# Optimization experiments

Measured on AMD Instinct MI355X. Metric: run time of the kernel, lower is better.

Reference implementation:

```python
import jax, jax.numpy as jnp
import numpy as np

EPS = 1e-05
NUM_SEGMENTS = 8  # number of point clouds packed along N


def setup_inputs() -> dict:
    key = jax.random.key(0)
    N, C = 1048576, 64
    seg_len = N // NUM_SEGMENTS
    x = jax.random.normal(key, (1, N, C), dtype=jnp.float32)
    # CSR offsets of equal-length contiguous segments: [0, L, 2L, ..., N]
    batch_offsets = (jnp.arange(NUM_SEGMENTS + 1, dtype=jnp.int32) * seg_len)
    # per-point segment id, consistent with offsets (segment-sorted)
    batch_indices = jnp.repeat(jnp.arange(NUM_SEGMENTS, dtype=jnp.int32), seg_len)
    weight = jnp.ones((C,), dtype=jnp.float32)
    bias_val = jnp.zeros((C,), dtype=jnp.float32)
    return {"x": x, "weight": weight, "bias_val": bias_val,
            "batch_offsets": batch_offsets, "batch_indices": batch_indices}


def reference(x, weight, bias_val, batch_offsets, batch_indices):
    # x: [B, N, C]; batch_offsets: [S+1]; batch_indices: [N]
    counts = (batch_offsets[1:] - batch_offsets[:-1]).astype(x.dtype)  # [S]

    def norm_one(xb):  # xb: [N, C]
        seg_mean = jax.ops.segment_sum(xb, batch_indices,
                                       num_segments=NUM_SEGMENTS) / counts[:, None]  # [S, C]
        centered = xb - seg_mean[batch_indices]                                      # [N, C]
        seg_var = jax.ops.segment_sum(centered * centered, batch_indices,
                                      num_segments=NUM_SEGMENTS) / counts[:, None]   # [S, C]
        std = jnp.sqrt(seg_var + EPS)                                                # [S, C]
        return centered / std[batch_indices]

    y = jax.vmap(norm_one)(x)  # [B, N, C]
    return y * weight + bias_val
```

## Files before the change

### kernel.cpp

```cpp
#include <hip/hip_runtime.h>
#include <hip/hip_bf16.h>


#define EPS 1e-5f

typedef float f32x4 __attribute__((ext_vector_type(4)));

__global__ __launch_bounds__(256) void pin_stats(
    const float4* __restrict__ x4, float* __restrict__ partials,
    int ppb, long N) {
    const int tid   = threadIdx.x;
    const int lane  = tid & 63;
    const int wave  = tid >> 6;
    const int cgrp  = lane & 15;
    const int quart = lane >> 4;
    const long bchunk = (long)gridDim.x - 1 - blockIdx.x;
    const long block_start = bchunk * ppb;

    float4 s = make_float4(0.f, 0.f, 0.f, 0.f);
    float4 q = make_float4(0.f, 0.f, 0.f, 0.f);

    const int iters = ppb >> 4;
    const long lane_base = (block_start + wave * 4 + quart) * 16 + cgrp;

    if (block_start + ppb <= N) {
        const int half = iters >> 1;
        float4 s1 = make_float4(0.f, 0.f, 0.f, 0.f);
        float4 q1 = make_float4(0.f, 0.f, 0.f, 0.f);
        #pragma unroll 4
        for (int it = 0; it < half; ++it) {
            float4 a = x4[lane_base + (long)it * 256];
            float4 b = x4[lane_base + (long)(it + half) * 256];
            s.x  += a.x; s.y  += a.y; s.z  += a.z; s.w  += a.w;
            q.x  += a.x * a.x; q.y  += a.y * a.y; q.z  += a.z * a.z; q.w  += a.w * a.w;
            s1.x += b.x; s1.y += b.y; s1.z += b.z; s1.w += b.w;
            q1.x += b.x * b.x; q1.y += b.y * b.y; q1.z += b.z * b.z; q1.w += b.w * b.w;
        }
        s.x += s1.x; s.y += s1.y; s.z += s1.z; s.w += s1.w;
        q.x += q1.x; q.y += q1.y; q.z += q1.z; q.w += q1.w;
    } else {
        for (int it = 0; it < iters; ++it) {
            long p = block_start + (long)it * 16 + wave * 4 + quart;
            if (p < N) {
                float4 v = x4[p * 16 + cgrp];
                s.x += v.x; s.y += v.y; s.z += v.z; s.w += v.w;
                q.x += v.x * v.x; q.y += v.y * v.y; q.z += v.z * v.z; q.w += v.w * v.w;
            }
        }
    }

    #pragma unroll
    for (int off = 16; off <= 32; off <<= 1) {
        s.x += __shfl_xor(s.x, off); s.y += __shfl_xor(s.y, off);
        s.z += __shfl_xor(s.z, off); s.w += __shfl_xor(s.w, off);
        q.x += __shfl_xor(q.x, off); q.y += __shfl_xor(q.y, off);
        q.z += __shfl_xor(q.z, off); q.w += __shfl_xor(q.w, off);
    }

    __shared__ float lds[4][16][8];
    if (lane < 16) {
        lds[wave][lane][0] = s.x; lds[wave][lane][1] = s.y;
        lds[wave][lane][2] = s.z; lds[wave][lane][3] = s.w;
        lds[wave][lane][4] = q.x; lds[wave][lane][5] = q.y;
        lds[wave][lane][6] = q.z; lds[wave][lane][7] = q.w;
    }
    __syncthreads();

    if (tid < 128) {
        int stat = tid >> 6;
        int ch   = tid & 63;
        int cg   = ch >> 2;
        int j    = ch & 3;
        float v = lds[0][cg][stat * 4 + j] + lds[1][cg][stat * 4 + j]
                + lds[2][cg][stat * 4 + j] + lds[3][cg][stat * 4 + j];
        partials[bchunk * 128 + tid] = v;
    }
}

__global__ __launch_bounds__(256) void pin_scale(
    const float* __restrict__ partials,
    const float* __restrict__ weight, const float* __restrict__ bias,
    const int* __restrict__ offs,
    float* __restrict__ scale, float* __restrict__ shift, int ppb) {
    const int s = blockIdx.x;
    const int c = threadIdx.x & 63;
    const int r = threadIdx.x >> 6;
    const int b0 = offs[s] / ppb;
    const int b1 = offs[s + 1] / ppb;

    float sum = 0.f, sq = 0.f;
    for (int blk = b0 + r; blk < b1; blk += 4) {
        sum += partials[(long)blk * 128 + c];
        sq  += partials[(long)blk * 128 + 64 + c];
    }

    __shared__ float lsum[4][64];
    __shared__ float lsq[4][64];
    lsum[r][c] = sum;
    lsq[r][c]  = sq;
    __syncthreads();

    if (r == 0) {
        float tsum = ((lsum[0][c] + lsum[1][c]) + lsum[2][c]) + lsum[3][c];
        float tsq  = ((lsq[0][c]  + lsq[1][c])  + lsq[2][c])  + lsq[3][c];
        float cnt  = (float)(offs[s + 1] - offs[s]);
        float mean = tsum / cnt;
        float var  = tsq / cnt - mean * mean;
        float sc   = weight[c] * rsqrtf(var + EPS);
        scale[s * 64 + c] = sc;
        shift[s * 64 + c] = bias[c] - mean * sc;
    }
}

#define K3_THREADS 256
#define K3_ITERS 16
__global__ __launch_bounds__(K3_THREADS) void pin_norm(
    const f32x4* __restrict__ x4, const int* __restrict__ bidx,
    const float4* __restrict__ scale4, const float4* __restrict__ shift4,
    f32x4* __restrict__ y4, long total4) {
    const long chunk = (long)blockIdx.x * (K3_THREADS * K3_ITERS);
    const int  tid   = threadIdx.x;
    const long p0    = chunk >> 4;
    const int  seg   = bidx[p0];
    const int  cgrp  = tid & 15;

    const float4 sc = scale4[seg * 16 + cgrp];
    const float4 sh = shift4[seg * 16 + cgrp];

    if (chunk + K3_THREADS * K3_ITERS <= total4) {
        #pragma unroll
        for (int k = 0; k < K3_ITERS; ++k) {
            long i = chunk + (long)k * K3_THREADS + tid;
            f32x4 v = x4[i];
            f32x4 o;
            o.x = v.x * sc.x + sh.x;
            o.y = v.y * sc.y + sh.y;
            o.z = v.z * sc.z + sh.z;
            o.w = v.w * sc.w + sh.w;
            __builtin_nontemporal_store(o, &y4[i]);
        }
    } else {
        for (int k = 0; k < K3_ITERS; ++k) {
            long i = chunk + (long)k * K3_THREADS + tid;
            if (i < total4) {
                f32x4 v = x4[i];
                f32x4 o;
                o.x = v.x * sc.x + sh.x;
                o.y = v.y * sc.y + sh.y;
                o.z = v.z * sc.z + sh.z;
                o.w = v.w * sc.w + sh.w;
                __builtin_nontemporal_store(o, &y4[i]);
            }
        }
    }
}

extern "C" void kernel_launch(void* const* d_in, const int* in_sizes, int n_in,
                              void* d_out, int out_size, void* d_ws, size_t ws_size,
                              hipStream_t stream) {
    const float* x       = (const float*)d_in[0];
    const float* weight  = (const float*)d_in[1];
    const float* bias    = (const float*)d_in[2];
    const int*   offs    = (const int*)d_in[3];
    const int*   bidx    = (const int*)d_in[4];
    float* out = (float*)d_out;

    const long C = in_sizes[1];
    const long N = (long)in_sizes[0] / C;
    const int  S = in_sizes[3] - 1;

    int ppb = 1024;
    long nb1;
    for (;;) {
        nb1 = (N + ppb - 1) / ppb;
        size_t need = (size_t)(nb1 * 128 + 2 * S * 64) * sizeof(float);
        if (need <= ws_size || ppb >= (1 << 20)) break;
        ppb <<= 1;
    }

    float* partials = (float*)d_ws;
    float* scale    = partials + nb1 * 128;
    float* shift    = scale + S * 64;

    pin_stats<<<(int)nb1, 256, 0, stream>>>((const float4*)x, partials, ppb, N);
    pin_scale<<<S, 256, 0, stream>>>(partials, weight, bias, offs, scale, shift, ppb);

    const long total4 = N * (C / 4);
    const long nb3 = (total4 + (K3_THREADS * K3_ITERS) - 1) / (K3_THREADS * K3_ITERS);
    pin_norm<<<(int)nb3, K3_THREADS, 0, stream>>>(
        (const f32x4*)x, bidx, (const float4*)scale, (const float4*)shift,
        (f32x4*)out, total4);
}
```

Baseline: 137.9 us.

## Partition stats kernel per segment with fixed blocks-per-segment and strided loads

Result: no change. 137.3 us (-0.4%).

```diff
diff --git a/kernel.cpp b/kernel.cpp
--- a/kernel.cpp
+++ b/kernel.cpp
@@ -8,40 +8,36 @@
 
 __global__ __launch_bounds__(256) void pin_stats(
     const float4* __restrict__ x4, float* __restrict__ partials,
-    int ppb, long N) {
+    const int* __restrict__ offs, int bps, long N) {
     const int tid   = threadIdx.x;
     const int lane  = tid & 63;
     const int wave  = tid >> 6;
     const int cgrp  = lane & 15;
     const int quart = lane >> 4;
-    const long bchunk = (long)gridDim.x - 1 - blockIdx.x;
-    const long block_start = bchunk * ppb;
+    const int bid   = blockIdx.x;
+    const int seg   = bid / bps;
+    const int sub   = bid - seg * bps;
+    const long seg_start = offs[seg];
+    const long seg_len   = (long)offs[seg + 1] - seg_start;
 
     float4 s = make_float4(0.f, 0.f, 0.f, 0.f);
     float4 q = make_float4(0.f, 0.f, 0.f, 0.f);
 
-    const int iters = ppb >> 4;
-    const long lane_base = (block_start + wave * 4 + quart) * 16 + cgrp;
-
-    if (block_start + ppb <= N) {
-        const int half = iters >> 1;
-        float4 s1 = make_float4(0.f, 0.f, 0.f, 0.f);
-        float4 q1 = make_float4(0.f, 0.f, 0.f, 0.f);
-        #pragma unroll 4
-        for (int it = 0; it < half; ++it) {
-            float4 a = x4[lane_base + (long)it * 256];
-            float4 b = x4[lane_base + (long)(it + half) * 256];
-            s.x  += a.x; s.y  += a.y; s.z  += a.z; s.w  += a.w;
-            q.x  += a.x * a.x; q.y  += a.y * a.y; q.z  += a.z * a.z; q.w  += a.w * a.w;
-            s1.x += b.x; s1.y += b.y; s1.z += b.z; s1.w += b.w;
-            q1.x += b.x * b.x; q1.y += b.y * b.y; q1.z += b.z * b.z; q1.w += b.w * b.w;
+    if (seg_len % ((long)bps * 16) == 0) {
+        const long my_iters = seg_len / ((long)bps * 16);
+        const long step4    = (long)bps * 256;
+        long addr = (seg_start + (long)sub * 16 + wave * 4 + quart) * 16 + cgrp;
+        #pragma unroll 8
+        for (long it = 0; it < my_iters; ++it) {
+            float4 v = x4[addr + it * step4];
+            s.x += v.x; s.y += v.y; s.z += v.z; s.w += v.w;
+            q.x += v.x * v.x; q.y += v.y * v.y; q.z += v.z * v.z; q.w += v.w * v.w;
         }
-        s.x += s1.x; s.y += s1.y; s.z += s1.z; s.w += s1.w;
-        q.x += q1.x; q.y += q1.y; q.z += q1.z; q.w += q1.w;
     } else {
-        for (int it = 0; it < iters; ++it) {
-            long p = block_start + (long)it * 16 + wave * 4 + quart;
-            if (p < N) {
+        const long iters_total = (seg_len + 15) >> 4;
+        for (long it = sub; it < iters_total; it += bps) {
+            long p = seg_start + it * 16 + wave * 4 + quart;
+            if (p < seg_start + seg_len && p < N) {
                 float4 v = x4[p * 16 + cgrp];
                 s.x += v.x; s.y += v.y; s.z += v.z; s.w += v.w;
                 q.x += v.x * v.x; q.y += v.y * v.y; q.z += v.z * v.z; q.w += v.w * v.w;
@@ -73,7 +69,7 @@
         int j    = ch & 3;
         float v = lds[0][cg][stat * 4 + j] + lds[1][cg][stat * 4 + j]
                 + lds[2][cg][stat * 4 + j] + lds[3][cg][stat * 4 + j];
-        partials[bchunk * 128 + tid] = v;
+        partials[(long)bid * 128 + tid] = v;
     }
 }
 
@@ -81,12 +77,12 @@
     const float* __restrict__ partials,
     const float* __restrict__ weight, const float* __restrict__ bias,
     const int* __restrict__ offs,
-    float* __restrict__ scale, float* __restrict__ shift, int ppb) {
+    float* __restrict__ scale, float* __restrict__ shift, int bps) {
     const int s = blockIdx.x;
     const int c = threadIdx.x & 63;
     const int r = threadIdx.x >> 6;
-    const int b0 = offs[s] / ppb;
-    const int b1 = offs[s + 1] / ppb;
+    const int b0 = s * bps;
+    const int b1 = b0 + bps;
 
     float sum = 0.f, sq = 0.f;
     for (int blk = b0 + r; blk < b1; blk += 4) {
@@ -169,21 +165,17 @@
     const long N = (long)in_sizes[0] / C;
     const int  S = in_sizes[3] - 1;
 
-    int ppb = 1024;
-    long nb1;
-    for (;;) {
-        nb1 = (N + ppb - 1) / ppb;
-        size_t need = (size_t)(nb1 * 128 + 2 * S * 64) * sizeof(float);
-        if (need <= ws_size || ppb >= (1 << 20)) break;
-        ppb <<= 1;
-    }
+    int bps = 128;
+    while ((size_t)((long)S * bps * 128 + 2 * S * 64) * sizeof(float) > ws_size
+           && bps > 8)
+        bps >>= 1;
 
     float* partials = (float*)d_ws;
-    float* scale    = partials + nb1 * 128;
+    float* scale    = partials + (long)S * bps * 128;
     float* shift    = scale + S * 64;
 
-    pin_stats<<<(int)nb1, 256, 0, stream>>>((const float4*)x, partials, ppb, N);
-    pin_scale<<<S, 256, 0, stream>>>(partials, weight, bias, offs, scale, shift, ppb);
+    pin_stats<<<S * bps, 256, 0, stream>>>((const float4*)x, partials, offs, bps, N);
+    pin_scale<<<S, 256, 0, stream>>>(partials, weight, bias, offs, scale, shift, bps);
 
     const long total4 = N * (C / 4);
     const long nb3 = (total4 + (K3_THREADS * K3_ITERS) - 1) / (K3_THREADS * K3_ITERS);
```
